# Kernel tuning notes

Hardware: AMD Instinct MI355X
Metric: run time of the kernel (lower is better)

Reference implementation:

```python
import jax, jax.numpy as jnp
import numpy as np

N_HEADS = 16


def _apply_rope(x, cos, sin):
    # x: [B, H, S, hd]; cos/sin: [>=S, hd/2]
    S = x.shape[2]
    cos = cos[None, None, :S]
    sin = sin[None, None, :S]
    x1, x2 = x[..., ::2], x[..., 1::2]
    # interleaved rotate, matching torch stack(...).flatten(-2)
    return jnp.stack([x1 * cos - x2 * sin, x1 * sin + x2 * cos], axis=-1).reshape(x.shape)


def setup_inputs() -> dict:
    key = jax.random.key(0)
    B, S, D = 2, 2048, 1024
    hd = D // N_HEADS
    k1, k2, k3 = jax.random.split(key, 3)
    x = jax.random.normal(k1, (B, S, D), dtype=jnp.float32)
    # standard RoPE tables (theta=10000)
    inv_freq = 1.0 / (10000.0 ** (np.arange(0, hd, 2, dtype=np.float32) / hd))  # [hd/2]
    freqs = np.outer(np.arange(S, dtype=np.float32), inv_freq)  # [S, hd/2]
    rope_cos = jnp.asarray(np.cos(freqs), dtype=jnp.float32)
    rope_sin = jnp.asarray(np.sin(freqs), dtype=jnp.float32)
    W_qkv = jax.random.normal(k2, (D, 3 * D), dtype=jnp.float32) * (D ** -0.5)
    W_out = jax.random.normal(k3, (D, D), dtype=jnp.float32) * (D ** -0.5)
    return {"x": x, "rope_cos": rope_cos, "rope_sin": rope_sin, "W_qkv": W_qkv, "W_out": W_out}


def reference(x, rope_cos, rope_sin, W_qkv, W_out):
    B, S, D = x.shape
    H = N_HEADS
    hd = D // H
    qkv = (x @ W_qkv).reshape(B, S, 3, H, hd)  # fused QKV projection
    q = qkv[:, :, 0].transpose(0, 2, 1, 3)  # [B,H,S,hd]
    k = qkv[:, :, 1].transpose(0, 2, 1, 3)
    v = qkv[:, :, 2].transpose(0, 2, 1, 3)
    q = _apply_rope(q, rope_cos, rope_sin)
    k = _apply_rope(k, rope_cos, rope_sin)
    scale = hd ** -0.5
    scores = jnp.einsum('bhqd,bhkd->bhqk', q, k) * scale  # [B,H,S,S]
    causal = jnp.tril(jnp.ones((S, S), dtype=bool))
    scores = jnp.where(causal, scores, jnp.finfo(scores.dtype).min)
    attn = jax.nn.softmax(scores, axis=-1)
    out = jnp.einsum('bhqk,bhkd->bhqd', attn, v)  # [B,H,S,hd]
    out = out.transpose(0, 2, 1, 3).reshape(B, S, D)
    return out @ W_out  # dropout is identity in eval mode
```

## Files before the change

kernel.cpp:

```cpp
#include <hip/hip_runtime.h>
#include <stdint.h>

typedef short bf16x8 __attribute__((ext_vector_type(8)));
typedef short bf16x4 __attribute__((ext_vector_type(4)));
typedef float f32x4 __attribute__((ext_vector_type(4)));

#define HD 64
#define NH 16
#define SEQ 2048
#define BATCH 2
#define DM 1024
#define TOK (BATCH * SEQ)

__device__ __forceinline__ unsigned short f2bf(float f) {
    union { float f; unsigned u; } a; a.f = f;
    unsigned r = a.u + 0x7fffu + ((a.u >> 16) & 1u);
    return (unsigned short)(r >> 16);
}
__device__ __forceinline__ float bf2f(unsigned short u) {
    union { unsigned u; float f; } a; a.u = ((unsigned)u) << 16;
    return a.f;
}

__device__ __forceinline__ float fexp2(float x) {
#if __has_builtin(__builtin_amdgcn_exp2f)
    return __builtin_amdgcn_exp2f(x);
#else
    return exp2f(x);
#endif
}
__device__ __forceinline__ float frcp(float x) {
#if __has_builtin(__builtin_amdgcn_rcpf)
    return __builtin_amdgcn_rcpf(x);
#else
    return 1.0f / x;
#endif
}

__device__ __forceinline__ f32x4 mfma16(bf16x4 a, bf16x4 b, f32x4 c) {
#if defined(__HIP_DEVICE_COMPILE__)
    return __builtin_amdgcn_mfma_f32_16x16x16bf16_1k(a, b, c, 0, 0, 0);
#else
    (void)a; (void)b;
    return c;
#endif
}

__device__ __forceinline__ void gld_lds16(const unsigned short* g, unsigned short* l) {
#if __has_builtin(__builtin_amdgcn_global_load_lds)
    __builtin_amdgcn_global_load_lds(
        (const __attribute__((address_space(1))) unsigned int*)g,
        (__attribute__((address_space(3))) unsigned int*)l, 16, 0, 0);
#else
    *(bf16x8*)l = *(const bf16x8*)g;
#endif
}

__global__ void __launch_bounds__(256) k_prep(const float* __restrict__ x,
                                              unsigned short* __restrict__ xb,
                                              const float* __restrict__ wqkv,
                                              unsigned short* __restrict__ wqkvt,
                                              const float* __restrict__ wout,
                                              unsigned short* __restrict__ woutt) {
    int bid = blockIdx.x;
    int tid = threadIdx.x;
    if (bid < 4096) {
        int i = (bid * 256 + tid) * 4;
        float4 v = *(const float4*)(x + i);
        union { ushort4 v; unsigned short s[4]; } o;
        o.s[0] = f2bf(v.x); o.s[1] = f2bf(v.y); o.s[2] = f2bf(v.z); o.s[3] = f2bf(v.w);
        *(ushort4*)(xb + i) = o.v;
        return;
    }
    const float* W; unsigned short* Wt; int N, t;
    if (bid < 7168) { W = wqkv; Wt = wqkvt; N = 3 * DM; t = bid - 4096; }
    else            { W = wout; Wt = woutt; N = DM;     t = bid - 7168; }
    int ntx = N >> 5;
    int bx = t % ntx, by = t / ntx;
    int tx = tid & 31, ty = tid >> 5;
    __shared__ float tile[32][33];
    for (int r = 0; r < 4; ++r) {
        int k = by * 32 + ty + r * 8;
        int n = bx * 32 + tx;
        tile[ty + r * 8][tx] = W[(size_t)k * N + n];
    }
    __syncthreads();
    for (int r = 0; r < 4; ++r) {
        int n = bx * 32 + ty + r * 8;
        int k = by * 32 + tx;
        Wt[(size_t)n * DM + k] = f2bf(tile[tx][ty + r * 8]);
    }
}

#define BKK 32

template <int MODE>
__device__ __forceinline__ void gemm_core(const unsigned short* __restrict__ A,
                                          const unsigned short* __restrict__ Bt,
                                          int K, int N,
                                          float* __restrict__ C,
                                          unsigned short* __restrict__ qbuf,
                                          unsigned short* __restrict__ kbuf,
                                          unsigned short* __restrict__ vt) {
    __shared__ unsigned short As0[128 * BKK];
    __shared__ unsigned short As1[128 * BKK];
    __shared__ unsigned short Bs0[128 * BKK];
    __shared__ unsigned short Bs1[128 * BKK];
    int tid = threadIdx.x;
    int lane = tid & 63, wave = tid >> 6;
    int row0 = blockIdx.y * 128;
    int col0 = blockIdx.x * 128;
    int wm = (wave >> 1) * 64, wn = (wave & 1) * 64;
    int fr = lane & 15;
    int quad = lane >> 4;

    f32x4 zero4 = {0.f, 0.f, 0.f, 0.f};
    f32x4 acc[4][4];
    for (int i = 0; i < 4; ++i)
        for (int j = 0; j < 4; ++j) acc[i][j] = zero4;

    auto stage = [&](unsigned short* Ad, unsigned short* Bd, int k0) {
        for (int i = 0; i < 2; ++i) {
            int s2 = i * 256 + tid;
            int r = s2 >> 2, kc = s2 & 3;
            int kk = (kc ^ (r & 3)) * 8;
            gld_lds16(A + (size_t)(row0 + r) * K + k0 + kk, Ad + (i * 256 + wave * 64) * 8);
            gld_lds16(Bt + (size_t)(col0 + r) * K + k0 + kk, Bd + (i * 256 + wave * 64) * 8);
        }
    };
    auto compute = [&](const unsigned short* Al, const unsigned short* Bl) {
        bf16x8 af[4], bf[4];
        for (int i = 0; i < 4; ++i) {
            int rr = wm + i * 16 + fr;
            af[i] = *(const bf16x8*)&Al[rr * BKK + ((quad ^ (rr & 3)) * 8)];
        }
        for (int j = 0; j < 4; ++j) {
            int rr = wn + j * 16 + fr;
            bf[j] = *(const bf16x8*)&Bl[rr * BKK + ((quad ^ (rr & 3)) * 8)];
        }
        for (int i = 0; i < 4; ++i)
            for (int j = 0; j < 4; ++j)
                acc[i][j] = __builtin_amdgcn_mfma_f32_16x16x32_bf16(af[i], bf[j], acc[i][j], 0, 0, 0);
    };

    stage(As0, Bs0, 0);
    __syncthreads();
    for (int k0 = 0; k0 < K; k0 += 2 * BKK) {
        if (k0 + BKK < K) stage(As1, Bs1, k0 + BKK);
        compute(As0, Bs0);
        __syncthreads();
        if (k0 + 2 * BKK < K) stage(As0, Bs0, k0 + 2 * BKK);
        compute(As1, Bs1);
        __syncthreads();
    }

    int rq = (lane >> 4) * 4;
    int cq = lane & 15;
    for (int i = 0; i < 4; ++i)
        for (int j = 0; j < 4; ++j)
            for (int reg = 0; reg < 4; ++reg) {
                int row = row0 + wm + i * 16 + rq + reg;
                int col = col0 + wn + j * 16 + cq;
                float v = acc[i][j][reg];
                if (MODE == 0) {
                    C[(size_t)row * N + col] = v;
                } else {
                    int which = col >> 10;
                    int hc = col & 1023;
                    int h = hc >> 6, d = hc & 63;
                    int b = row >> 11, s = row & (SEQ - 1);
                    int bh = b * NH + h;
                    unsigned short bv = f2bf(v);
                    if (which == 0)      qbuf[((size_t)bh * SEQ + s) * HD + d] = bv;
                    else if (which == 1) kbuf[((size_t)bh * SEQ + s) * HD + d] = bv;
                    else                 vt[((size_t)bh * HD + d) * SEQ + s] = bv;
                }
            }
}

__global__ void __launch_bounds__(256) k_gemm_qkv(const unsigned short* __restrict__ A,
                                                  const unsigned short* __restrict__ Bt,
                                                  unsigned short* __restrict__ qbuf,
                                                  unsigned short* __restrict__ kbuf,
                                                  unsigned short* __restrict__ vt) {
    gemm_core<1>(A, Bt, DM, 3 * DM, nullptr, qbuf, kbuf, vt);
}

__global__ void __launch_bounds__(256) k_gemm_out(const unsigned short* __restrict__ A,
                                                  const unsigned short* __restrict__ Bt,
                                                  float* __restrict__ C) {
    gemm_core<0>(A, Bt, DM, DM, C, nullptr, nullptr, nullptr);
}

__global__ void k_rope(unsigned short* __restrict__ qbuf, unsigned short* __restrict__ kbuf,
                       const float* __restrict__ cosb, const float* __restrict__ sinb) {
    int t = blockIdx.x * 256 + threadIdx.x;
    int c = t & 7;
    int row = (t >> 3) & 65535;
    int which = t >> 19;
    unsigned short* p = (which ? kbuf : qbuf) + (size_t)row * HD + c * 8;
    float sc = which ? 1.0f : (0.125f * 1.44269504f);
    int s = row & (SEQ - 1);
    const float* cs = cosb + s * 32 + c * 4;
    const float* sn = sinb + s * 32 + c * 4;
    bf16x8 v = *(const bf16x8*)p;
    bf16x8 o;
    for (int i = 0; i < 4; ++i) {
        float x1 = bf2f((unsigned short)v[2 * i]);
        float x2 = bf2f((unsigned short)v[2 * i + 1]);
        float cc = cs[i], ss = sn[i];
        o[2 * i]     = (short)f2bf((x1 * cc - x2 * ss) * sc);
        o[2 * i + 1] = (short)f2bf((x1 * ss + x2 * cc) * sc);
    }
    *(bf16x8*)p = o;
}

__global__ void __launch_bounds__(256, 4) k_attn(const unsigned short* __restrict__ qbuf,
                                                 const unsigned short* __restrict__ kbuf,
                                                 const unsigned short* __restrict__ vt,
                                                 unsigned short* __restrict__ obuf) {
    __shared__ unsigned short Ks0[64 * 64];
    __shared__ unsigned short Ks1[64 * 64];
    __shared__ unsigned short Vs0[64 * 64];
    __shared__ unsigned short Vs1[64 * 64];

    int tid = threadIdx.x;
    int lane = tid & 63, wave = tid >> 6;
    int bh = blockIdx.y;
    int b = bh >> 4, h = bh & 15;
    int qt = (int)gridDim.x - 1 - (int)blockIdx.x;
    int qb = qt * 64;
    int fr = lane & 15, quad = lane >> 4;
    int Qmin = qb + wave * 16;

    const unsigned short* Qb = qbuf + (size_t)bh * SEQ * HD;
    const unsigned short* Kb = kbuf + (size_t)bh * SEQ * HD;
    const unsigned short* Vb = vt + (size_t)bh * HD * SEQ;

    int qrow = Qmin + fr;
    bf16x8 qf0 = *(const bf16x8*)(Qb + (size_t)qrow * HD + quad * 8);
    bf16x8 qf1 = *(const bf16x8*)(Qb + (size_t)qrow * HD + 32 + quad * 8);

    f32x4 zero4 = {0.f, 0.f, 0.f, 0.f};
    f32x4 o[4];
    for (int j = 0; j < 4; ++j) o[j] = zero4;
    float l = 0.f;

    auto stage = [&](int kb, unsigned short* Kd, unsigned short* Vd) {
        for (int a = 0; a < 2; ++a) {
            int idx = a * 256 + tid;
            int r = idx >> 3;
            int lg = (idx & 7) ^ (r & 7);
            gld_lds16(Kb + (size_t)(kb + r) * HD + lg * 8, Kd + (a * 256 + wave * 64) * 8);
            gld_lds16(Vb + (size_t)r * SEQ + kb + lg * 8, Vd + (a * 256 + wave * 64) * 8);
        }
    };

    auto compute = [&](int kt, const unsigned short* Kd, const unsigned short* Vd) {
        int kb = kt * 64;
        int sw = fr & 7;
        f32x4 sg[4];
        for (int g = 0; g < 4; ++g) {
            int r = g * 16 + fr;
            bf16x8 ka = *(const bf16x8*)&Kd[r * 64 + ((quad ^ sw) * 8)];
            bf16x8 kc = *(const bf16x8*)&Kd[r * 64 + (((quad + 4) ^ sw) * 8)];
            f32x4 z = zero4;
            z = __builtin_amdgcn_mfma_f32_16x16x32_bf16(ka, qf0, z, 0, 0, 0);
            z = __builtin_amdgcn_mfma_f32_16x16x32_bf16(kc, qf1, z, 0, 0, 0);
            sg[g] = z;
        }
        if (kt == qt) {
            int q = Qmin + fr;
            for (int g = 0; g < 4; ++g)
                for (int reg = 0; reg < 4; ++reg)
                    if (kb + g * 16 + quad * 4 + reg > q) sg[g][reg] = -1e30f;
        }
        bf16x4 pf[4];
        for (int g = 0; g < 4; ++g) {
            float ps = 0.f;
            bf16x4 pk;
            for (int reg = 0; reg < 4; ++reg) {
                float p = fexp2(sg[g][reg]);
                ps += p;
                pk[reg] = (short)f2bf(p);
            }
            pf[g] = pk;
            l += ps;
        }
        for (int g = 0; g < 4; ++g)
            for (int db = 0; db < 4; ++db) {
                int d = db * 16 + fr;
                int pg = ((2 * g + (quad >> 1)) ^ sw) * 8 + (quad & 1) * 4;
                bf16x4 vf = *(const bf16x4*)&Vd[d * 64 + pg];
                o[db] = mfma16(pf[g], vf, o[db]);
            }
    };

    stage(0, Ks0, Vs0);
    __syncthreads();
    for (int kt = 0; kt <= qt; kt += 2) {
        if (kt + 1 <= qt) stage((kt + 1) * 64, Ks1, Vs1);
        compute(kt, Ks0, Vs0);
        __syncthreads();
        if (kt + 1 <= qt) {
            if (kt + 2 <= qt) stage((kt + 2) * 64, Ks0, Vs0);
            compute(kt + 1, Ks1, Vs1);
            __syncthreads();
        }
    }

    l += __shfl_xor(l, 16);
    l += __shfl_xor(l, 32);
    float linv[4];
    for (int reg = 0; reg < 4; ++reg)
        linv[reg] = frcp(__shfl(l, quad * 4 + reg));

    for (int db = 0; db < 4; ++db)
        for (int reg = 0; reg < 4; ++reg) {
            int s = Qmin + quad * 4 + reg;
            int d = db * 16 + fr;
            obuf[((size_t)(b * SEQ + s)) * DM + h * HD + d] = f2bf(o[db][reg] * linv[reg]);
        }
}

extern "C" void kernel_launch(void* const* d_in, const int* in_sizes, int n_in,
                              void* d_out, int out_size, void* d_ws, size_t ws_size,
                              hipStream_t stream) {
    const float* x    = (const float*)d_in[0];
    const float* rc   = (const float*)d_in[1];
    const float* rs   = (const float*)d_in[2];
    const float* wqkv = (const float*)d_in[3];
    const float* wout = (const float*)d_in[4];
    float* out = (float*)d_out;

    char* ws = (char*)d_ws;
    size_t off = 0;
    auto alloc = [&](size_t bytes) {
        char* p = ws + off;
        off += (bytes + 255) & ~(size_t)255;
        return p;
    };
    unsigned short* xb    = (unsigned short*)alloc((size_t)TOK * DM * 2);
    unsigned short* wqkvt = (unsigned short*)alloc((size_t)3 * DM * DM * 2);
    unsigned short* woutt = (unsigned short*)alloc((size_t)DM * DM * 2);
    unsigned short* qbuf  = (unsigned short*)alloc((size_t)BATCH * NH * SEQ * HD * 2);
    unsigned short* kbuf  = (unsigned short*)alloc((size_t)BATCH * NH * SEQ * HD * 2);
    unsigned short* vtb   = (unsigned short*)alloc((size_t)BATCH * NH * SEQ * HD * 2);
    unsigned short* obuf  = (unsigned short*)alloc((size_t)TOK * DM * 2);

    k_prep<<<8192, 256, 0, stream>>>(x, xb, wqkv, wqkvt, wout, woutt);
    k_gemm_qkv<<<dim3(3 * DM / 128, TOK / 128), 256, 0, stream>>>(xb, wqkvt, qbuf, kbuf, vtb);
    k_rope<<<4096, 256, 0, stream>>>(qbuf, kbuf, rc, rs);
    k_attn<<<dim3(SEQ / 64, BATCH * NH), 256, 0, stream>>>(qbuf, kbuf, vtb, obuf);
    k_gemm_out<<<dim3(DM / 128, TOK / 128), 256, 0, stream>>>(obuf, woutt, out);
}
```

Baseline: 199.8 us.

## Fuse RoPE into QKV GEMM epilogue and pack bf16 conversions in attention

```diff
diff --git a/kernel.cpp b/kernel.cpp
--- a/kernel.cpp
+++ b/kernel.cpp
@@ -1,4 +1,5 @@
 #include <hip/hip_runtime.h>
+#include <hip/hip_bf16.h>
 #include <stdint.h>
 
 typedef short bf16x8 __attribute__((ext_vector_type(8)));
@@ -20,6 +21,12 @@
 __device__ __forceinline__ float bf2f(unsigned short u) {
     union { unsigned u; float f; } a; a.u = ((unsigned)u) << 16;
     return a.f;
+}
+
+__device__ __forceinline__ unsigned pkbf16(float a, float b) {
+    union { __hip_bfloat162 h; unsigned u; } cv;
+    cv.h = __float22bfloat162_rn(make_float2(a, b));
+    return cv.u;
 }
 
 __device__ __forceinline__ float fexp2(float x) {
@@ -101,7 +108,9 @@
                                           float* __restrict__ C,
                                           unsigned short* __restrict__ qbuf,
                                           unsigned short* __restrict__ kbuf,
-                                          unsigned short* __restrict__ vt) {
+                                          unsigned short* __restrict__ vt,
+                                          const float* __restrict__ cosb,
+                                          const float* __restrict__ sinb) {
     __shared__ unsigned short As0[128 * BKK];
     __shared__ unsigned short As1[128 * BKK];
     __shared__ unsigned short Bs0[128 * BKK];
@@ -156,6 +165,7 @@
 
     int rq = (lane >> 4) * 4;
     int cq = lane & 15;
+    const float qsc = 0.125f * 1.44269504f;
     for (int i = 0; i < 4; ++i)
         for (int j = 0; j < 4; ++j)
             for (int reg = 0; reg < 4; ++reg) {
@@ -165,12 +175,21 @@
                 if (MODE == 0) {
                     C[(size_t)row * N + col] = v;
                 } else {
+                    float pv = __shfl_xor(v, 1);
                     int which = col >> 10;
                     int hc = col & 1023;
                     int h = hc >> 6, d = hc & 63;
                     int b = row >> 11, s = row & (SEQ - 1);
                     int bh = b * NH + h;
-                    unsigned short bv = f2bf(v);
+                    float outv = v;
+                    if (which < 2) {
+                        float cc = cosb[s * 32 + (d >> 1)];
+                        float ss = sinb[s * 32 + (d >> 1)];
+                        if (col & 1) outv = pv * ss + v * cc;
+                        else         outv = v * cc - pv * ss;
+                        if (which == 0) outv *= qsc;
+                    }
+                    unsigned short bv = f2bf(outv);
                     if (which == 0)      qbuf[((size_t)bh * SEQ + s) * HD + d] = bv;
                     else if (which == 1) kbuf[((size_t)bh * SEQ + s) * HD + d] = bv;
                     else                 vt[((size_t)bh * HD + d) * SEQ + s] = bv;
@@ -182,37 +201,16 @@
                                                   const unsigned short* __restrict__ Bt,
                                                   unsigned short* __restrict__ qbuf,
                                                   unsigned short* __restrict__ kbuf,
-                                                  unsigned short* __restrict__ vt) {
-    gemm_core<1>(A, Bt, DM, 3 * DM, nullptr, qbuf, kbuf, vt);
+                                                  unsigned short* __restrict__ vt,
+                                                  const float* __restrict__ cosb,
+                                                  const float* __restrict__ sinb) {
+    gemm_core<1>(A, Bt, DM, 3 * DM, nullptr, qbuf, kbuf, vt, cosb, sinb);
 }
 
 __global__ void __launch_bounds__(256) k_gemm_out(const unsigned short* __restrict__ A,
                                                   const unsigned short* __restrict__ Bt,
                                                   float* __restrict__ C) {
-    gemm_core<0>(A, Bt, DM, DM, C, nullptr, nullptr, nullptr);
-}
-
-__global__ void k_rope(unsigned short* __restrict__ qbuf, unsigned short* __restrict__ kbuf,
-                       const float* __restrict__ cosb, const float* __restrict__ sinb) {
-    int t = blockIdx.x * 256 + threadIdx.x;
-    int c = t & 7;
-    int row = (t >> 3) & 65535;
-    int which = t >> 19;
-    unsigned short* p = (which ? kbuf : qbuf) + (size_t)row * HD + c * 8;
-    float sc = which ? 1.0f : (0.125f * 1.44269504f);
-    int s = row & (SEQ - 1);
-    const float* cs = cosb + s * 32 + c * 4;
-    const float* sn = sinb + s * 32 + c * 4;
-    bf16x8 v = *(const bf16x8*)p;
-    bf16x8 o;
-    for (int i = 0; i < 4; ++i) {
-        float x1 = bf2f((unsigned short)v[2 * i]);
-        float x2 = bf2f((unsigned short)v[2 * i + 1]);
-        float cc = cs[i], ss = sn[i];
-        o[2 * i]     = (short)f2bf((x1 * cc - x2 * ss) * sc);
-        o[2 * i + 1] = (short)f2bf((x1 * ss + x2 * cc) * sc);
-    }
-    *(bf16x8*)p = o;
+    gemm_core<0>(A, Bt, DM, DM, C, nullptr, nullptr, nullptr, nullptr, nullptr);
 }
 
 __global__ void __launch_bounds__(256, 4) k_attn(const unsigned short* __restrict__ qbuf,
@@ -277,15 +275,15 @@
         }
         bf16x4 pf[4];
         for (int g = 0; g < 4; ++g) {
-            float ps = 0.f;
-            bf16x4 pk;
-            for (int reg = 0; reg < 4; ++reg) {
-                float p = fexp2(sg[g][reg]);
-                ps += p;
-                pk[reg] = (short)f2bf(p);
-            }
-            pf[g] = pk;
-            l += ps;
+            float p0 = fexp2(sg[g][0]);
+            float p1 = fexp2(sg[g][1]);
+            float p2 = fexp2(sg[g][2]);
+            float p3 = fexp2(sg[g][3]);
+            l += (p0 + p1) + (p2 + p3);
+            union { bf16x4 v; unsigned u[2]; } pc;
+            pc.u[0] = pkbf16(p0, p1);
+            pc.u[1] = pkbf16(p2, p3);
+            pf[g] = pc.v;
         }
         for (int g = 0; g < 4; ++g)
             for (int db = 0; db < 4; ++db) {
@@ -349,8 +347,7 @@
     unsigned short* obuf  = (unsigned short*)alloc((size_t)TOK * DM * 2);
 
     k_prep<<<8192, 256, 0, stream>>>(x, xb, wqkv, wqkvt, wout, woutt);
-    k_gemm_qkv<<<dim3(3 * DM / 128, TOK / 128), 256, 0, stream>>>(xb, wqkvt, qbuf, kbuf, vtb);
-    k_rope<<<4096, 256, 0, stream>>>(qbuf, kbuf, rc, rs);
+    k_gemm_qkv<<<dim3(3 * DM / 128, TOK / 128), 256, 0, stream>>>(xb, wqkvt, qbuf, kbuf, vtb, rc, rs);
     k_attn<<<dim3(SEQ / 64, BATCH * NH), 256, 0, stream>>>(qbuf, kbuf, vtb, obuf);
     k_gemm_out<<<dim3(DM / 128, TOK / 128), 256, 0, stream>>>(obuf, woutt, out);
 }
```

After: 222.9 us. +11.5%, slower.
